# Kernel optimization log

Hardware: AMD Instinct MI355X
Metric: run time of the kernel (lower is better)

The kernel has to match this reference:

```python
import jax, jax.numpy as jnp
import numpy as np

NUM_HEADS = 8
NEG_SLOPE = 0.2


def setup_inputs() -> dict:
    key = jax.random.key(0)
    k1, k2, k3, k4 = jax.random.split(key, 4)
    B, N, D_IN, D_K, D_V = 4, 4096, 256, 256, 256
    x = jax.random.normal(k1, (B, N, D_IN), dtype=jnp.float32)
    Wq = jax.random.normal(k2, (D_IN, D_K), dtype=jnp.float32) * (1.0 / np.sqrt(D_IN))
    Wk = jax.random.normal(k3, (D_IN, D_K), dtype=jnp.float32) * (1.0 / np.sqrt(D_IN))
    Wv = jax.random.normal(k4, (D_IN, D_V), dtype=jnp.float32) * (1.0 / np.sqrt(D_IN))
    return {"x": x, "Wq": Wq, "Wk": Wk, "Wv": Wv}


def reference(x, Wq, Wk, Wv):
    B, N, _ = x.shape
    nh = NUM_HEADS
    dim_k = Wq.shape[1]
    dim_v = Wv.shape[1]
    dk, dv = dim_k // nh, dim_v // nh
    nor_fact = 1.0 / np.sqrt(dk)
    # project and split heads: [B, H, N, dk]
    q = (x @ Wq).reshape(B, N, nh, dk).transpose(0, 2, 1, 3)
    k = (x @ Wk).reshape(B, N, nh, dk).transpose(0, 2, 1, 3)
    v = (x @ Wv).reshape(B, N, nh, dv).transpose(0, 2, 1, 3)
    # all-pairs scores, scaled then LeakyReLU (no softmax)
    dist = jnp.einsum('bhnd,bhmd->bhnm', q, k) * nor_fact
    dist = jnp.where(dist >= 0, dist, NEG_SLOPE * dist)
    att = jnp.einsum('bhnm,bhmd->bhnd', dist, v)
    return att.transpose(0, 2, 1, 3).reshape(B, N, dim_v)
```

## Files before the change

### kernel.cpp

```cpp
#include <hip/hip_runtime.h>

typedef __attribute__((ext_vector_type(8))) short short8;
typedef __attribute__((ext_vector_type(4))) short short4v;
typedef __attribute__((ext_vector_type(4))) float f32x4;
typedef __attribute__((ext_vector_type(2))) unsigned int u32x2;

#define MFMA16x32(A, B, C) \
  __builtin_amdgcn_mfma_f32_16x16x32_bf16((A), (B), (C), 0, 0, 0)

#if defined(__has_builtin)
#if __has_builtin(__builtin_amdgcn_mfma_f32_16x16x16bf16_1k)
#define HAVE_MFMA_1K 1
#endif
#endif

__device__ __forceinline__ f32x4 mfma16x16(short4v a, short4v b, f32x4 c) {
#ifdef HAVE_MFMA_1K
  return __builtin_amdgcn_mfma_f32_16x16x16bf16_1k(a, b, c, 0, 0, 0);
#else
  f32x4 d;
  asm("v_mfma_f32_16x16x16_bf16 %0, %1, %2, %3"
      : "=v"(d)
      : "v"(a), "v"(b), "v"(c));
  return d;
#endif
}

__device__ __forceinline__ void async_cp16(const unsigned short* g, void* l) {
  __builtin_amdgcn_global_load_lds(
      (const __attribute__((address_space(1))) unsigned int*)g,
      (__attribute__((address_space(3))) unsigned int*)l, 16, 0, 0);
}

__device__ __forceinline__ unsigned int fbits(float f) {
  return __builtin_bit_cast(unsigned int, f);
}
__device__ __forceinline__ unsigned int pack_bf16(float a, float b) {
  return __builtin_amdgcn_perm(fbits(b), fbits(a), 0x07060302u);
}
__device__ __forceinline__ unsigned short bf16_rne(float f) {
  unsigned int u = fbits(f);
  return (unsigned short)((u + 0x8000u) >> 16);
}

__global__ __launch_bounds__(256) void xconv_kernel(
    const float* __restrict__ x, unsigned short* __restrict__ xb) {
  const size_t i = ((size_t)blockIdx.x * 256 + threadIdx.x) * 4;
  const float4 f = *(const float4*)(x + i);
  u32x2 u = {(unsigned int)bf16_rne(f.x) | ((unsigned int)bf16_rne(f.y) << 16),
             (unsigned int)bf16_rne(f.z) | ((unsigned int)bf16_rne(f.w) << 16)};
  *(u32x2*)(xb + i) = u;
}

__global__ __launch_bounds__(256) void wtrans_kernel(
    const float* __restrict__ Wq, const float* __restrict__ Wk,
    const float* __restrict__ Wv, unsigned short* __restrict__ WT) {
  __shared__ float tile[32][33];
  const int bid = blockIdx.x;
  const int g = bid / 64, rem = bid % 64;
  const int k0 = (rem >> 3) * 32, n0 = (rem & 7) * 32;
  const float* W = (g == 0) ? Wq : (g == 1) ? Wk : Wv;
  const int t = threadIdx.x;
  {
    const int kr = t >> 3, nc = (t & 7) * 4;
    const float4 f = *(const float4*)(W + (size_t)(k0 + kr) * 256 + n0 + nc);
    tile[kr][nc + 0] = f.x; tile[kr][nc + 1] = f.y;
    tile[kr][nc + 2] = f.z; tile[kr][nc + 3] = f.w;
  }
  __syncthreads();
  {
    const int nr = t >> 3, kc = (t & 7) * 4;
    unsigned int u0 = (unsigned int)bf16_rne(tile[kc + 0][nr]) |
                      ((unsigned int)bf16_rne(tile[kc + 1][nr]) << 16);
    unsigned int u1 = (unsigned int)bf16_rne(tile[kc + 2][nr]) |
                      ((unsigned int)bf16_rne(tile[kc + 3][nr]) << 16);
    u32x2 u = {u0, u1};
    *(u32x2*)(WT + (size_t)g * 65536 + (size_t)(n0 + nr) * 256 + k0 + kc) = u;
  }
}

__global__ __launch_bounds__(256, 2) void proj_kernel(
    const unsigned short* __restrict__ xb, const unsigned short* __restrict__ WT,
    unsigned short* __restrict__ QH, unsigned short* __restrict__ KH,
    unsigned short* __restrict__ VT) {
  __shared__ __align__(16) char smem[65536];
  const int tid = threadIdx.x;
  const int w = tid >> 6, lane = tid & 63, l15 = lane & 15, quad = lane >> 4;
  const int bid = blockIdx.x;
  const int mtile = bid / 6, nt = bid % 6;
  const int g = nt >> 1, n0 = (nt & 1) * 128;
  const int m0 = mtile * 128;

  const int srow = lane >> 3, useg = lane & 7;
  const int swz = (useg ^ srow) * 8;
  const unsigned short* aS = xb + (size_t)(m0 + w * 32 + srow) * 256 + swz;
  const unsigned short* bS =
      WT + (size_t)g * 65536 + (size_t)(n0 + w * 32 + srow) * 256 + swz;

#pragma unroll
  for (int j = 0; j < 4; j++) {
    async_cp16(aS + j * 2048, smem + w * 4096 + j * 1024);
    async_cp16(bS + j * 2048, smem + 16384 + w * 4096 + j * 1024);
  }
  __syncthreads();

  const f32x4 zero = {0.f, 0.f, 0.f, 0.f};
  f32x4 acc[2][8];
#pragma unroll
  for (int s = 0; s < 2; s++)
#pragma unroll
    for (int c = 0; c < 8; c++) acc[s][c] = zero;

  const int sw = l15 & 7;
  for (int t = 0; t < 4; t++) {
    const int nb = t & 1;
    const int kn = ((t + 1) & 3) * 64;
#pragma unroll
    for (int j = 0; j < 4; j++) {
      async_cp16(aS + kn + j * 2048,
                 smem + (nb ^ 1) * 32768 + w * 4096 + j * 1024);
      async_cp16(bS + kn + j * 2048,
                 smem + (nb ^ 1) * 32768 + 16384 + w * 4096 + j * 1024);
    }
    const char* Ab = smem + nb * 32768;
    const char* Bb = Ab + 16384;
#pragma unroll
    for (int ks = 0; ks < 2; ks++) {
      const int seg = ((ks * 4 + quad) ^ sw) * 16;
      short8 af[2], bf[8];
#pragma unroll
      for (int s = 0; s < 2; s++)
        af[s] = *(const short8*)(Ab + (w * 32 + s * 16 + l15) * 128 + seg);
#pragma unroll
      for (int c = 0; c < 8; c++)
        bf[c] = *(const short8*)(Bb + (c * 16 + l15) * 128 + seg);
      if (g < 2) {
#pragma unroll
        for (int s = 0; s < 2; s++)
#pragma unroll
          for (int c = 0; c < 8; c++)
            acc[s][c] = MFMA16x32(bf[c], af[s], acc[s][c]);
      } else {
#pragma unroll
        for (int s = 0; s < 2; s++)
#pragma unroll
          for (int c = 0; c < 8; c++)
            acc[s][c] = MFMA16x32(af[s], bf[c], acc[s][c]);
      }
    }
    __syncthreads();
  }

  if (g < 2) {
    unsigned short* O = g ? KH : QH;
    const float sc = g ? 1.0f : 0.17677669529663688f;
#pragma unroll
    for (int s = 0; s < 2; s++)
#pragma unroll
      for (int c = 0; c < 8; c++) {
        const int row = m0 + w * 32 + s * 16 + l15;
        const int col = n0 + c * 16 + quad * 4;
        const int bb = row >> 12, nn = row & 4095;
        const int hh = col >> 5, dl = col & 31;
        u32x2 pk = {pack_bf16(acc[s][c][0] * sc, acc[s][c][1] * sc),
                    pack_bf16(acc[s][c][2] * sc, acc[s][c][3] * sc)};
        *(u32x2*)(O + ((size_t)(bb * 8 + hh) * 4096 + nn) * 32 + dl) = pk;
      }
  } else {
#pragma unroll
    for (int s = 0; s < 2; s++)
#pragma unroll
      for (int c = 0; c < 8; c++) {
        const int col = n0 + c * 16 + l15;
        const int hh = col >> 5, dl = col & 31;
        const int row = m0 + w * 32 + s * 16 + quad * 4;
        const int bb = row >> 12, nn = row & 4095;
        u32x2 pk = {pack_bf16(acc[s][c][0], acc[s][c][1]),
                    pack_bf16(acc[s][c][2], acc[s][c][3])};
        *(u32x2*)(VT + (size_t)((bb * 8 + hh) * 32 + dl) * 4096 + nn) = pk;
      }
  }
}

__global__ __launch_bounds__(512, 2) void attn_kernel(
    const unsigned short* __restrict__ QH, const unsigned short* __restrict__ KH,
    const unsigned short* __restrict__ VT, float* __restrict__ out) {
  __shared__ __align__(16) char smem[16384];
  const int tid = threadIdx.x;
  const int w = tid >> 6, lane = tid & 63, l15 = lane & 15, quad = lane >> 4;
  const int bid = blockIdx.x;
  const int bh = bid & 31, qh = bid >> 5;
  const int b = bh >> 3, h = bh & 7;
  const int qbase = qh * 512 + w * 64;

  const unsigned short* Qp =
      QH + ((size_t)bh * 4096 + qbase + l15) * 32 + quad * 8;
  short8 qf[4];
#pragma unroll
  for (int s = 0; s < 4; s++) qf[s] = *(const short8*)(Qp + (size_t)s * 512);

  const bool isK = (w < 4);
  const unsigned short* src0;
  int kstr, wbOff;
  if (isK) {
    const int key = w * 16 + (lane >> 2), dseg = lane & 3;
    src0 = KH + ((size_t)bh * 4096 + key) * 32 + dseg * 8;
    kstr = 32;
    wbOff = w * 1024;
  } else {
    const int r = (w - 4) * 8 + (lane >> 3), useg = lane & 7;
    src0 = VT + ((size_t)bh * 32 + r) * 4096 + ((useg ^ (r & 7)) * 8);
    kstr = 1;
    wbOff = 4096 + (w - 4) * 1024;
  }

  async_cp16(src0, smem + wbOff);
  __syncthreads();

  const f32x4 zero = {0.f, 0.f, 0.f, 0.f};
  f32x4 acc[4][2];
#pragma unroll
  for (int s = 0; s < 4; s++) {
    acc[s][0] = zero;
    acc[s][1] = zero;
  }

  const int rs = l15 & 7;
  for (int i = 0; i < 64; i++) {
    const int nb = i & 1;
    const int kn = ((i + 1) & 63) * 64;
    async_cp16(src0 + (size_t)kn * kstr, smem + (nb ^ 1) * 8192 + wbOff);

    const char* Kb = smem + nb * 8192;
    const char* Vb = Kb + 4096;
    short8 kf[4];
#pragma unroll
    for (int c = 0; c < 4; c++)
      kf[c] = *(const short8*)(Kb + (c * 16 + l15) * 64 + quad * 16);
    short4v vf[2][4];
#pragma unroll
    for (int dt = 0; dt < 2; dt++) {
      const char* Vr = Vb + (dt * 16 + l15) * 128 + (quad & 1) * 8;
#pragma unroll
      for (int c = 0; c < 4; c++) {
        const int tt = c * 2 + (quad >> 1);
        vf[dt][c] = *(const short4v*)(Vr + ((tt ^ rs) * 16));
      }
    }

#pragma unroll
    for (int s = 0; s < 4; s++) {
#pragma unroll
      for (int c = 0; c < 4; c++) {
        f32x4 st = MFMA16x32(kf[c], qf[s], zero);
        float t0 = fmaxf(st[0], 0.2f * st[0]);
        float t1 = fmaxf(st[1], 0.2f * st[1]);
        float t2 = fmaxf(st[2], 0.2f * st[2]);
        float t3 = fmaxf(st[3], 0.2f * st[3]);
        u32x2 pk = {pack_bf16(t0, t1), pack_bf16(t2, t3)};
        const short4v pb = __builtin_bit_cast(short4v, pk);
#pragma unroll
        for (int dt = 0; dt < 2; dt++)
          acc[s][dt] = mfma16x16(vf[dt][c], pb, acc[s][dt]);
      }
    }
    __syncthreads();
  }

#pragma unroll
  for (int s = 0; s < 4; s++)
#pragma unroll
    for (int dt = 0; dt < 2; dt++)
      *(f32x4*)(out + ((size_t)b * 4096 + qbase + s * 16 + l15) * 256 + h * 32 +
                dt * 16 + quad * 4) = acc[s][dt];
}

extern "C" void kernel_launch(void* const* d_in, const int* in_sizes, int n_in,
                              void* d_out, int out_size, void* d_ws,
                              size_t ws_size, hipStream_t stream) {
  const float* x = (const float*)d_in[0];
  const float* Wq = (const float*)d_in[1];
  const float* Wk = (const float*)d_in[2];
  const float* Wv = (const float*)d_in[3];
  float* out = (float*)d_out;

  unsigned short* ws = (unsigned short*)d_ws;
  unsigned short* QHb = ws;
  unsigned short* KHb = ws + 4194304;
  unsigned short* VTb = ws + 2 * 4194304;
  unsigned short* xbb = ws + 3 * 4194304;
  unsigned short* WTb = ws + 4 * 4194304;

  xconv_kernel<<<4096, 256, 0, stream>>>(x, xbb);
  wtrans_kernel<<<192, 256, 0, stream>>>(Wq, Wk, Wv, WTb);
  proj_kernel<<<768, 256, 0, stream>>>(xbb, WTb, QHb, KHb, VTb);
  attn_kernel<<<256, 512, 0, stream>>>(QHb, KHb, VTb, out);
}
```

Baseline: 175.7 us.

## Use 16x16x32 MFMA for PV, swizzle K in LDS, merge prep kernels

The P·V product now uses the 16x16x32 bf16 MFMA instead of two 16x16x16 instructions. To make that possible, the V^T store in the projection kernel permutes the key order within each 32-key group so that each lane's 8 contiguous keys line up with the packed score fragments. K tiles in LDS are XOR-swizzled by segment to reduce bank conflicts on fragment reads, and V fragments are read as 16-byte loads. The x conversion and weight transpose kernels are merged into one launch to save launch overhead. The risk is that the key permutation in V^T must match the score lane layout exactly.

```diff
diff --git a/kernel.cpp b/kernel.cpp
--- a/kernel.cpp
+++ b/kernel.cpp
@@ -1,30 +1,12 @@
 #include <hip/hip_runtime.h>
 
 typedef __attribute__((ext_vector_type(8))) short short8;
-typedef __attribute__((ext_vector_type(4))) short short4v;
 typedef __attribute__((ext_vector_type(4))) float f32x4;
 typedef __attribute__((ext_vector_type(2))) unsigned int u32x2;
+typedef __attribute__((ext_vector_type(4))) unsigned int u32x4;
 
 #define MFMA16x32(A, B, C) \
   __builtin_amdgcn_mfma_f32_16x16x32_bf16((A), (B), (C), 0, 0, 0)
-
-#if defined(__has_builtin)
-#if __has_builtin(__builtin_amdgcn_mfma_f32_16x16x16bf16_1k)
-#define HAVE_MFMA_1K 1
-#endif
-#endif
-
-__device__ __forceinline__ f32x4 mfma16x16(short4v a, short4v b, f32x4 c) {
-#ifdef HAVE_MFMA_1K
-  return __builtin_amdgcn_mfma_f32_16x16x16bf16_1k(a, b, c, 0, 0, 0);
-#else
-  f32x4 d;
-  asm("v_mfma_f32_16x16x16_bf16 %0, %1, %2, %3"
-      : "=v"(d)
-      : "v"(a), "v"(b), "v"(c));
-  return d;
-#endif
-}
 
 __device__ __forceinline__ void async_cp16(const unsigned short* g, void* l) {
   __builtin_amdgcn_global_load_lds(
@@ -43,20 +25,20 @@
   return (unsigned short)((u + 0x8000u) >> 16);
 }
 
-__global__ __launch_bounds__(256) void xconv_kernel(
-    const float* __restrict__ x, unsigned short* __restrict__ xb) {
-  const size_t i = ((size_t)blockIdx.x * 256 + threadIdx.x) * 4;
-  const float4 f = *(const float4*)(x + i);
-  u32x2 u = {(unsigned int)bf16_rne(f.x) | ((unsigned int)bf16_rne(f.y) << 16),
-             (unsigned int)bf16_rne(f.z) | ((unsigned int)bf16_rne(f.w) << 16)};
-  *(u32x2*)(xb + i) = u;
-}
-
-__global__ __launch_bounds__(256) void wtrans_kernel(
+__global__ __launch_bounds__(256) void prep_kernel(
+    const float* __restrict__ x, unsigned short* __restrict__ xb,
     const float* __restrict__ Wq, const float* __restrict__ Wk,
     const float* __restrict__ Wv, unsigned short* __restrict__ WT) {
   __shared__ float tile[32][33];
-  const int bid = blockIdx.x;
+  if (blockIdx.x < 4096) {
+    const size_t i = ((size_t)blockIdx.x * 256 + threadIdx.x) * 4;
+    const float4 f = *(const float4*)(x + i);
+    u32x2 u = {(unsigned int)bf16_rne(f.x) | ((unsigned int)bf16_rne(f.y) << 16),
+               (unsigned int)bf16_rne(f.z) | ((unsigned int)bf16_rne(f.w) << 16)};
+    *(u32x2*)(xb + i) = u;
+    return;
+  }
+  const int bid = blockIdx.x - 4096;
   const int g = bid / 64, rem = bid % 64;
   const int k0 = (rem >> 3) * 32, n0 = (rem & 7) * 32;
   const float* W = (g == 0) ? Wq : (g == 1) ? Wk : Wv;
@@ -174,7 +156,8 @@
         const int col = n0 + c * 16 + l15;
         const int hh = col >> 5, dl = col & 31;
         const int row = m0 + w * 32 + s * 16 + quad * 4;
-        const int bb = row >> 12, nn = row & 4095;
+        const int bb = row >> 12;
+        const int nn = (row & 4064) | (quad << 3) | ((s & 1) << 2);
         u32x2 pk = {pack_bf16(acc[s][c][0], acc[s][c][1]),
                     pack_bf16(acc[s][c][2], acc[s][c][3])};
         *(u32x2*)(VT + (size_t)((bb * 8 + hh) * 32 + dl) * 4096 + nn) = pk;
@@ -203,8 +186,9 @@
   const unsigned short* src0;
   int kstr, wbOff;
   if (isK) {
-    const int key = w * 16 + (lane >> 2), dseg = lane & 3;
-    src0 = KH + ((size_t)bh * 4096 + key) * 32 + dseg * 8;
+    const int key = w * 16 + (lane >> 2);
+    const int gseg = (lane & 3) ^ ((lane >> 3) & 3);
+    src0 = KH + ((size_t)bh * 4096 + key) * 32 + gseg * 8;
     kstr = 32;
     wbOff = w * 1024;
   } else {
@@ -226,6 +210,7 @@
   }
 
   const int rs = l15 & 7;
+  const int kseg = (quad ^ ((l15 >> 1) & 3)) * 16;
   for (int i = 0; i < 64; i++) {
     const int nb = i & 1;
     const int kn = ((i + 1) & 63) * 64;
@@ -236,20 +221,19 @@
     short8 kf[4];
 #pragma unroll
     for (int c = 0; c < 4; c++)
-      kf[c] = *(const short8*)(Kb + (c * 16 + l15) * 64 + quad * 16);
-    short4v vf[2][4];
+      kf[c] = *(const short8*)(Kb + (c * 16 + l15) * 64 + kseg);
+    short8 vf[2][2];
 #pragma unroll
     for (int dt = 0; dt < 2; dt++) {
-      const char* Vr = Vb + (dt * 16 + l15) * 128 + (quad & 1) * 8;
-#pragma unroll
-      for (int c = 0; c < 4; c++) {
-        const int tt = c * 2 + (quad >> 1);
-        vf[dt][c] = *(const short4v*)(Vr + ((tt ^ rs) * 16));
-      }
+      const char* Vr = Vb + (dt * 16 + l15) * 128;
+#pragma unroll
+      for (int u = 0; u < 2; u++)
+        vf[dt][u] = *(const short8*)(Vr + (((4 * u + quad) ^ rs) * 16));
     }
 
 #pragma unroll
     for (int s = 0; s < 4; s++) {
+      unsigned int pp[4][2];
 #pragma unroll
       for (int c = 0; c < 4; c++) {
         f32x4 st = MFMA16x32(kf[c], qf[s], zero);
@@ -257,11 +241,17 @@
         float t1 = fmaxf(st[1], 0.2f * st[1]);
         float t2 = fmaxf(st[2], 0.2f * st[2]);
         float t3 = fmaxf(st[3], 0.2f * st[3]);
-        u32x2 pk = {pack_bf16(t0, t1), pack_bf16(t2, t3)};
-        const short4v pb = __builtin_bit_cast(short4v, pk);
+        pp[c][0] = pack_bf16(t0, t1);
+        pp[c][1] = pack_bf16(t2, t3);
+      }
+#pragma unroll
+      for (int u = 0; u < 2; u++) {
+        u32x4 bw = {pp[2 * u][0], pp[2 * u][1],
+                    pp[2 * u + 1][0], pp[2 * u + 1][1]};
+        short8 pb = __builtin_bit_cast(short8, bw);
 #pragma unroll
         for (int dt = 0; dt < 2; dt++)
-          acc[s][dt] = mfma16x16(vf[dt][c], pb, acc[s][dt]);
+          acc[s][dt] = MFMA16x32(vf[dt][u], pb, acc[s][dt]);
       }
     }
     __syncthreads();
@@ -291,8 +281,7 @@
   unsigned short* xbb = ws + 3 * 4194304;
   unsigned short* WTb = ws + 4 * 4194304;
 
-  xconv_kernel<<<4096, 256, 0, stream>>>(x, xbb);
-  wtrans_kernel<<<192, 256, 0, stream>>>(Wq, Wk, Wv, WTb);
+  prep_kernel<<<4288, 256, 0, stream>>>(x, xbb, Wq, Wk, Wv, WTb);
   proj_kernel<<<768, 256, 0, stream>>>(xbb, WTb, QHb, KHb, VTb);
   attn_kernel<<<256, 512, 0, stream>>>(QHb, KHb, VTb, out);
 }
```

After: 172.6 us. Within noise of the previous version (-1.8%).
